# Kernel tuning notes

Measured on AMD Instinct MI355X. Metric: run time of the kernel, lower is better.

The kernel has to match this reference:

```python
import jax, jax.numpy as jnp
import numpy as np

NUM_EMBED = 8192
EMBED_DIM = 256


def setup_inputs() -> dict:
    key = jax.random.key(0)
    k1, k2 = jax.random.split(key)
    input_data = jax.random.normal(k1, (32, EMBED_DIM, 32, 32), dtype=jnp.float32)
    codebook = jax.random.normal(k2, (NUM_EMBED, EMBED_DIM), dtype=jnp.float32)
    return {"input_data": input_data, "codebook": codebook}


def reference(input_data, codebook):
    N, C, H, W = input_data.shape
    # NCHW -> NHWC -> [N*H*W, C]
    data = jnp.transpose(input_data, (0, 2, 3, 1)).reshape(-1, C)
    dist = (
        jnp.sum(data * data, axis=1, keepdims=True)          # [T, 1]
        - 2.0 * jnp.einsum("tc,kc->tk", data, codebook)      # [T, K]
        + jnp.sum(codebook * codebook, axis=1)[None, :]       # [1, K]
    )
    embed_ind = jnp.argmin(dist, axis=1)                      # [T]
    quantize = codebook[embed_ind]                            # [T, C] gather
    quantize_detach = data + jax.lax.stop_gradient(quantize - data)
    return quantize, quantize_detach, data
```

## Files before the change

kernel.cpp:

```cpp
#include <hip/hip_runtime.h>
#include <stdint.h>


#define T_TOT 32768
#define K_TOT 8192
#define CD    256
#define SPLITS 4
#define NSPLIT 2048
#define MT    64
#define NTI   32

typedef _Float16 h8 __attribute__((ext_vector_type(8)));
typedef _Float16 h4 __attribute__((ext_vector_type(4)));
typedef _Float16 h2 __attribute__((ext_vector_type(2)));
typedef float f4 __attribute__((ext_vector_type(4)));
typedef unsigned long long u64;
typedef unsigned int u32;

#define WS_AP    0u
#define WS_BP    16777216u
#define WS_E2    20971520u
#define WS_E2B   21004288u
#define WS_CAND  21037056u
#define WS_NEED  23265280u

__device__ __forceinline__ u64 shfl_xor_u64(u64 v, int off, int w) {
  unsigned lo = (unsigned)v, hi = (unsigned)(v >> 32);
  lo = __shfl_xor(lo, off, w);
  hi = __shfl_xor(hi, off, w);
  return ((u64)hi << 32) | lo;
}
__device__ __forceinline__ u64 umin64(u64 a, u64 b) { return a < b ? a : b; }
__device__ __forceinline__ u64 umax64(u64 a, u64 b) { return a < b ? b : a; }
__device__ __forceinline__ u32 umin32(u32 a, u32 b) { return a < b ? a : b; }
__device__ __forceinline__ u32 umax32(u32 a, u32 b) { return a < b ? b : a; }



__global__ __launch_bounds__(256) void cvt_data_kernel(
    const float* __restrict__ in, _Float16* __restrict__ Ap) {
  __shared__ float Ds[32][257];
  const int tid = threadIdx.x;
  const int t0 = blockIdx.x * 32;
  const int nbase = (t0 >> 10) << 18;
  const int tin = t0 & 1023;
  #pragma unroll 8
  for (int p = 0; p < 32; ++p) {
    const int lin = p * 256 + tid;
    const int cc = lin >> 5, tt = lin & 31;
    Ds[tt][cc] = in[nbase + cc * 1024 + tin + tt];
  }
  __syncthreads();
  const u64 g0 = (u64)(t0 >> 4);
  #pragma unroll
  for (int p = 0; p < 4; ++p) {
    const int id = p * 256 + tid;
    const int gl = id >> 9, kk = (id >> 6) & 7, l = id & 63;
    const int row = gl * 16 + (l & 15);
    const int c0 = kk * 32 + (l >> 4) * 8;
    h8 hv;
    #pragma unroll
    for (int j = 0; j < 8; ++j) hv[j] = (_Float16)(-Ds[row][c0 + j]);
    *(h8*)(Ap + ((g0 + (u64)gl) * 8 + kk) * 512 + (u64)l * 8) = hv;
  }
}

__global__ __launch_bounds__(256) void cvt_cb_kernel(
    const float* __restrict__ cb, _Float16* __restrict__ Bp,
    float* __restrict__ e2, float* __restrict__ e2b) {
  __shared__ float Cs[16][260];
  const int tid = threadIdx.x;
  const int g = blockIdx.x;
  #pragma unroll
  for (int r = 0; r < 16; ++r)
    Cs[r][tid] = cb[((u64)g * 16 + r) * 256 + tid];
  __syncthreads();
  const int w = tid >> 6, lane = tid & 63;
  #pragma unroll
  for (int rr = 0; rr < 4; ++rr) {
    const int row = w * 4 + rr;
    const float4 v = *(const float4*)&Cs[row][lane * 4];
    float s = v.x * v.x + v.y * v.y + v.z * v.z + v.w * v.w;
    #pragma unroll
    for (int off = 32; off >= 1; off >>= 1) s += __shfl_xor(s, off, 64);
    if (lane == 0) {
      e2[g * 16 + row] = s;
      e2b[g * 16 + row] = 0.5f * s + 256.0f;
    }
  }
  #pragma unroll
  for (int p = 0; p < 2; ++p) {
    const int id = p * 256 + tid;
    const int kk = id >> 6, l = id & 63;
    const int row = l & 15, c0 = kk * 32 + (l >> 4) * 8;
    h8 hv;
    #pragma unroll
    for (int j = 0; j < 8; ++j) hv[j] = (_Float16)Cs[row][c0 + j];
    *(h8*)(Bp + ((u64)g * 8 + kk) * 512 + (u64)l * 8) = hv;
  }
}

__global__ __launch_bounds__(256, 2) void screen_kernel(
    const _Float16* __restrict__ Ap, const _Float16* __restrict__ Bp,
    const float* __restrict__ e2b, u64* __restrict__ cand) {
  __shared__ u64 mbuf[4][64][2];

  const int tid = threadIdx.x;
  const int lane = tid & 63;
  const int w = tid >> 6;
  const int q = lane >> 4;
  const int c15 = lane & 15;

  const int bm = blockIdx.x & 511;
  const int split = blockIdx.x >> 9;
  const int t0 = bm * MT;
  const int n0s = split * NSPLIT;

  const h8* ap = (const h8*)Ap + (u64)(t0 >> 4) * 512 + lane;
  h8 af[4][8];
  #pragma unroll
  for (int mi = 0; mi < 4; ++mi)
    #pragma unroll
    for (int kk = 0; kk < 8; ++kk)
      af[mi][kk] = ap[(mi * 8 + kk) * 64];

  const h8* bp = (const h8*)Bp + ((u64)(n0s >> 4) + (u64)w) * 512 + lane;
  h8 bf[8];
  #pragma unroll
  for (int kk = 0; kk < 8; ++kk) bf[kk] = bp[kk * 64];

  const float* e2p = e2b + n0s + w * 16 + c15;
  float ev = e2p[0];

  u32 m1[16], m2[16];
  #pragma unroll
  for (int r = 0; r < 16; ++r) { m1[r] = 0xffffffffu; m2[r] = 0xffffffffu; }

  #pragma unroll 1
  for (int nt = 0; nt < NTI; ++nt) {
    const int ntn = (nt < NTI - 1) ? nt + 1 : nt;
    const float evn = e2p[ntn * 64];
    const h8* bn = bp + (u64)ntn * 2048;
    f4 acc[4];
    #pragma unroll
    for (int mi = 0; mi < 4; ++mi) acc[mi] = (f4){ev, ev, ev, ev};
    #pragma unroll
    for (int kk = 0; kk < 8; ++kk) {
      const h8 b = bf[kk];
      acc[0] = __builtin_amdgcn_mfma_f32_16x16x32_f16(af[0][kk], b, acc[0], 0, 0, 0);
      acc[1] = __builtin_amdgcn_mfma_f32_16x16x32_f16(af[1][kk], b, acc[1], 0, 0, 0);
      acc[2] = __builtin_amdgcn_mfma_f32_16x16x32_f16(af[2][kk], b, acc[2], 0, 0, 0);
      acc[3] = __builtin_amdgcn_mfma_f32_16x16x32_f16(af[3][kk], b, acc[3], 0, 0, 0);
      bf[kk] = bn[kk * 64];
    }
    #pragma unroll
    for (int mi = 0; mi < 4; ++mi)
      #pragma unroll
      for (int reg = 0; reg < 4; ++reg) {
        const int r = mi * 4 + reg;
        const u32 k = (__float_as_uint(acc[mi][reg]) & ~63u) | (u32)nt;
        const u32 t = umax32(m1[r], k);
        m1[r] = umin32(m1[r], k);
        m2[r] = umin32(m2[r], t);
      }
    ev = evn;
  }

  u64 P1[16], P2[16];
  #pragma unroll
  for (int r = 0; r < 16; ++r) {
    const u32 l1 = m1[r] & 63u, l2 = m2[r] & 63u;
    const u32 col1 = (u32)(n0s + (int)l1 * 64 + w * 16 + c15);
    const u32 col2 = (u32)(n0s + (int)l2 * 64 + w * 16 + c15);
    P1[r] = ((u64)m1[r] << 32) | col1;
    P2[r] = ((u64)m2[r] << 32) | col2;
  }
  #pragma unroll
  for (int st = 1; st < 16; st <<= 1) {
    #pragma unroll
    for (int r = 0; r < 16; ++r) {
      const u64 o1 = shfl_xor_u64(P1[r], st, 16);
      const u64 o2 = shfl_xor_u64(P2[r], st, 16);
      const u64 n1 = umin64(P1[r], o1);
      const u64 hi = umax64(P1[r], o1);
      P2[r] = umin64(hi, umin64(P2[r], o2));
      P1[r] = n1;
    }
  }
  if (c15 == 0) {
    #pragma unroll
    for (int r = 0; r < 16; ++r) {
      const int mi = r >> 2, reg = r & 3;
      const int row = mi * 16 + q * 4 + reg;
      mbuf[w][row][0] = P1[r];
      mbuf[w][row][1] = P2[r];
    }
  }
  __syncthreads();
  if (tid < 64) {
    const u64 a1 = mbuf[0][tid][0], a2 = mbuf[0][tid][1];
    const u64 b1 = mbuf[1][tid][0], b2 = mbuf[1][tid][1];
    const u64 c1 = mbuf[2][tid][0], c2 = mbuf[2][tid][1];
    const u64 d1 = mbuf[3][tid][0], d2 = mbuf[3][tid][1];
    const u64 x1 = umin64(a1, b1);
    const u64 x2 = umin64(umax64(a1, b1), umin64(a2, b2));
    const u64 y1 = umin64(c1, d1);
    const u64 y2 = umin64(umax64(c1, d1), umin64(c2, d2));
    const u64 n1 = umin64(x1, y1);
    const u64 n2 = umin64(umax64(x1, y1), umin64(x2, y2));
    cand[(u64)(t0 + tid) * 8 + split * 2 + 0] = n1;
    cand[(u64)(t0 + tid) * 8 + split * 2 + 1] = n2;
  }
}

__global__ __launch_bounds__(256) void rescore_output_kernel(
    const float* __restrict__ in, const float* __restrict__ cb,
    const float* __restrict__ e2, const u64* __restrict__ cand,
    float* __restrict__ out) {
  __shared__ __align__(16) float Ds[32][260];
  __shared__ int idxs[32];
  const int tid = threadIdx.x;
  const int t0 = blockIdx.x * 32;
  const int nbase = (t0 >> 10) << 18;
  const int tin = t0 & 1023;
  #pragma unroll 8
  for (int p = 0; p < 32; ++p) {
    const int lin = p * 256 + tid;
    const int cc = lin >> 5, tt = lin & 31;
    Ds[tt][cc] = in[nbase + cc * 1024 + tin + tt];
  }
  __syncthreads();
  const int w = tid >> 6, lane = tid & 63;
  for (int s = 0; s < 8; ++s) {
    const int tt = w * 8 + s;
    const int t = t0 + tt;
    int colv = 0;
    if (lane < 8) colv = (int)(u32)cand[(u64)t * 8 + lane];
    const float4 x = *(const float4*)&Ds[tt][lane * 4];
    float bestd = 1e30f; int bestc = 0x7fffffff;
    #pragma unroll
    for (int j = 0; j < 8; ++j) {
      const int col = __shfl(colv, j, 64);
      const float4 e = *(const float4*)(cb + (u64)col * CD + lane * 4);
      float p4 = x.x * e.x + x.y * e.y + x.z * e.z + x.w * e.w;
      #pragma unroll
      for (int off = 32; off >= 1; off >>= 1) p4 += __shfl_xor(p4, off, 64);
      const float d = e2[col] - 2.0f * p4;
      if (d < bestd || (d == bestd && col < bestc)) { bestd = d; bestc = col; }
    }
    if (lane == 0) idxs[tt] = bestc;
  }
  __syncthreads();
  float* out1 = out;
  float* out2 = out + 8388608;
  float* out3 = out + 16777216;
  for (int tt = 0; tt < 32; ++tt) {
    const float d = Ds[tt][tid];
    const int k = idxs[tt];
    const float qv = cb[k * CD + tid];
    const float qd = d + (qv - d);
    const int o = (t0 + tt) * CD + tid;
    out1[o] = qv;
    out2[o] = qd;
    out3[o] = d;
  }
}


__global__ __launch_bounds__(256) void norms_kernel(const float* __restrict__ in,
                                                    const float* __restrict__ cb,
                                                    float* __restrict__ e2,
                                                    float* __restrict__ x2) {
  const int b = blockIdx.x;
  const int tid = threadIdx.x;
  if (b < 2048) {
    const int wave = tid >> 6, lane = tid & 63;
    const int row = b * 4 + wave;
    const float4 v = *(const float4*)(cb + row * CD + lane * 4);
    float s = v.x * v.x + v.y * v.y + v.z * v.z + v.w * v.w;
    #pragma unroll
    for (int off = 32; off >= 1; off >>= 1) s += __shfl_down(s, off, 64);
    if (lane == 0) e2[row] = s;
  } else {
    const int t = (b - 2048) * 256 + tid;
    const float* p = in + ((t >> 10) << 18) + (t & 1023);
    float s = 0.f;
    #pragma unroll 8
    for (int c = 0; c < CD; ++c) { const float v = p[c << 10]; s += v * v; }
    x2[t] = s;
  }
}

__global__ __launch_bounds__(256) void dist_argmin_kernel(
    const float* __restrict__ in, const float* __restrict__ cb,
    const float* __restrict__ e2, const float* __restrict__ x2,
    u64* __restrict__ packed) {
  __shared__ __align__(16) float As_[32][128];
  __shared__ __align__(16) float Bs_[32][128];
  const int tid = threadIdx.x;
  const int tx = tid & 15, ty = tid >> 4;
  const int tb = blockIdx.x & 255;
  const int ks = blockIdx.x >> 8;
  const int t0 = tb * 128;
  const int nbase = (t0 >> 10) << 18;
  const int tin = t0 & 1023;
  float xi[8];
  #pragma unroll
  for (int i = 0; i < 8; ++i)
    xi[i] = x2[t0 + ty * 4 + (i & 3) + ((i >> 2) << 6)];
  u64 best[8];
  #pragma unroll
  for (int i = 0; i < 8; ++i) best[i] = ~0ull;
  for (int kt = 0; kt < 32; ++kt) {
    const int k0 = ks * 4096 + kt * 128;
    float acc[8][8];
    #pragma unroll
    for (int i = 0; i < 8; ++i)
      #pragma unroll
      for (int j = 0; j < 8; ++j) acc[i][j] = 0.f;
    float ej[8];
    #pragma unroll
    for (int j = 0; j < 8; ++j)
      ej[j] = e2[k0 + tx * 4 + (j & 3) + ((j >> 2) << 6)];
    for (int ch = 0; ch < 8; ++ch) {
      const int c0 = ch * 32;
      #pragma unroll
      for (int p = 0; p < 4; ++p) {
        const int l = p * 1024 + tid * 4;
        const int cc = l >> 7, tt = l & 127;
        *(float4*)&As_[cc][tt] =
            *(const float4*)(in + nbase + (c0 + cc) * 1024 + tin + tt);
      }
      #pragma unroll
      for (int p = 0; p < 4; ++p) {
        const int ix = p * 256 + tid;
        const int kk = ix >> 3, cs = (ix & 7) * 4;
        const float4 v = *(const float4*)(cb + (k0 + kk) * CD + c0 + cs);
        Bs_[cs + 0][kk] = v.x; Bs_[cs + 1][kk] = v.y;
        Bs_[cs + 2][kk] = v.z; Bs_[cs + 3][kk] = v.w;
      }
      __syncthreads();
      #pragma unroll
      for (int cc = 0; cc < 32; ++cc) {
        const float4 a0 = *(const float4*)&As_[cc][ty * 4];
        const float4 a1 = *(const float4*)&As_[cc][64 + ty * 4];
        const float4 b0 = *(const float4*)&Bs_[cc][tx * 4];
        const float4 b1 = *(const float4*)&Bs_[cc][64 + tx * 4];
        const float a[8]  = {a0.x, a0.y, a0.z, a0.w, a1.x, a1.y, a1.z, a1.w};
        const float bb[8] = {b0.x, b0.y, b0.z, b0.w, b1.x, b1.y, b1.z, b1.w};
        #pragma unroll
        for (int i = 0; i < 8; ++i)
          #pragma unroll
          for (int j = 0; j < 8; ++j)
            acc[i][j] += a[i] * bb[j];
      }
      __syncthreads();
    }
    #pragma unroll
    for (int i = 0; i < 8; ++i) {
      u64 m = best[i];
      #pragma unroll
      for (int j = 0; j < 8; ++j) {
        const float dist = (xi[i] - 2.0f * acc[i][j]) + ej[j];
        const int kidx = k0 + tx * 4 + (j & 3) + ((j >> 2) << 6);
        const u64 pk = ((u64)__float_as_uint(dist) << 32) | (unsigned)kidx;
        m = pk < m ? pk : m;
      }
      best[i] = m;
    }
  }
  #pragma unroll
  for (int i = 0; i < 8; ++i) {
    u64 m = best[i];
    #pragma unroll
    for (int off = 8; off >= 1; off >>= 1) {
      const u64 o = shfl_xor_u64(m, off, 16);
      m = o < m ? o : m;
    }
    if (tx == 0)
      atomicMin(&packed[t0 + ty * 4 + (i & 3) + ((i >> 2) << 6)], m);
  }
}

__global__ __launch_bounds__(256) void output_kernel(
    const float* __restrict__ in, const float* __restrict__ cb,
    const u64* __restrict__ packed, float* __restrict__ out) {
  __shared__ float Ds[32][257];
  __shared__ int idxs[32];
  const int tid = threadIdx.x;
  const int t0 = blockIdx.x * 32;
  const int nbase = (t0 >> 10) << 18;
  const int tin = t0 & 1023;
  if (tid < 32) idxs[tid] = (int)(packed[t0 + tid] & 0xffffffffull);
  #pragma unroll 8
  for (int p = 0; p < 32; ++p) {
    const int lin = p * 256 + tid;
    const int cc = lin >> 5, tt = lin & 31;
    Ds[tt][cc] = in[nbase + cc * 1024 + tin + tt];
  }
  __syncthreads();
  float* out1 = out;
  float* out2 = out + 8388608;
  float* out3 = out + 16777216;
  for (int tt = 0; tt < 32; ++tt) {
    const float d = Ds[tt][tid];
    const int k = idxs[tt];
    const float q = cb[k * CD + tid];
    const float qd = d + (q - d);
    const int o = (t0 + tt) * CD + tid;
    out1[o] = q;
    out2[o] = qd;
    out3[o] = d;
  }
}

extern "C" void kernel_launch(void* const* d_in, const int* in_sizes, int n_in,
                              void* d_out, int out_size, void* d_ws, size_t ws_size,
                              hipStream_t stream) {
  const float* in = (const float*)d_in[0];
  const float* cb = (const float*)d_in[1];
  float* out = (float*)d_out;

  if (ws_size >= WS_NEED) {
    _Float16* Ap = (_Float16*)((char*)d_ws + WS_AP);
    _Float16* Bp = (_Float16*)((char*)d_ws + WS_BP);
    float* e2  = (float*)((char*)d_ws + WS_E2);
    float* e2b = (float*)((char*)d_ws + WS_E2B);
    u64* cand  = (u64*)((char*)d_ws + WS_CAND);

    cvt_data_kernel<<<T_TOT / 32, 256, 0, stream>>>(in, Ap);
    cvt_cb_kernel<<<K_TOT / 16, 256, 0, stream>>>(cb, Bp, e2, e2b);
    screen_kernel<<<(T_TOT / MT) * SPLITS, 256, 0, stream>>>(Ap, Bp, e2b, cand);
    rescore_output_kernel<<<T_TOT / 32, 256, 0, stream>>>(in, cb, e2, cand, out);
  } else {
    u64* packed = (u64*)d_ws;
    float* e2 = (float*)((char*)d_ws + 262144);
    float* x2 = (float*)((char*)d_ws + 294912);
    hipMemsetAsync(packed, 0xFF, T_TOT * sizeof(u64), stream);
    norms_kernel<<<2176, 256, 0, stream>>>(in, cb, e2, x2);
    dist_argmin_kernel<<<512, 256, 0, stream>>>(in, cb, e2, x2, packed);
    output_kernel<<<T_TOT / 32, 256, 0, stream>>>(in, cb, packed, out);
  }
}
```

Measured before the change: 404.4 us.

## Stage codebook tiles via async global_load_lds double buffering in screen kernel

The screen kernel now loads codebook B fragments and the e2 bias into LDS with global_load_lds. Each wave double-buffers its 16-column tile and prefetches two iterations ahead, replacing the direct register prefetch from global memory. Block indices are also remapped so the four splits of neighbouring row tiles run adjacently, which should improve L2 reuse of A and B. The change adds LDS traffic and hand-placed waitcnt and sched_barrier instructions, and it reuses the B buffer for the final reduction. Correctness depends on the manual vmcnt accounting being right.

```diff
diff --git a/kernel.cpp b/kernel.cpp
--- a/kernel.cpp
+++ b/kernel.cpp
@@ -34,6 +34,19 @@
 __device__ __forceinline__ u64 umax64(u64 a, u64 b) { return a < b ? b : a; }
 __device__ __forceinline__ u32 umin32(u32 a, u32 b) { return a < b ? a : b; }
 __device__ __forceinline__ u32 umax32(u32 a, u32 b) { return a < b ? b : a; }
+
+__device__ __forceinline__ void gll16(const void* g, void* l) {
+  __builtin_amdgcn_global_load_lds(
+      (const __attribute__((address_space(1))) void*)g,
+      (__attribute__((address_space(3))) void*)l, 16, 0, 0);
+}
+
+__device__ __forceinline__ void stage_b(const _Float16* __restrict__ gsrc,
+                                        _Float16* ldst, int lane) {
+  #pragma unroll
+  for (int kk = 0; kk < 8; ++kk)
+    gll16(gsrc + kk * 512 + lane * 8, ldst + kk * 512);
+}
 
 
 
@@ -103,7 +116,8 @@
 __global__ __launch_bounds__(256, 2) void screen_kernel(
     const _Float16* __restrict__ Ap, const _Float16* __restrict__ Bp,
     const float* __restrict__ e2b, u64* __restrict__ cand) {
-  __shared__ u64 mbuf[4][64][2];
+  __shared__ __align__(16) _Float16 bsm[4][2][4096];
+  __shared__ __align__(16) float e2s[2048];
 
   const int tid = threadIdx.x;
   const int lane = tid & 63;
@@ -111,8 +125,10 @@
   const int q = lane >> 4;
   const int c15 = lane & 15;
 
-  const int bm = blockIdx.x & 511;
-  const int split = blockIdx.x >> 9;
+  const int x = blockIdx.x & 7;
+  const int m = blockIdx.x >> 3;
+  const int split = x >> 1;
+  const int bm = m * 2 + (x & 1);
   const int t0 = bm * MT;
   const int n0s = split * NSPLIT;
 
@@ -124,35 +140,44 @@
     for (int kk = 0; kk < 8; ++kk)
       af[mi][kk] = ap[(mi * 8 + kk) * 64];
 
-  const h8* bp = (const h8*)Bp + ((u64)(n0s >> 4) + (u64)w) * 512 + lane;
-  h8 bf[8];
-  #pragma unroll
-  for (int kk = 0; kk < 8; ++kk) bf[kk] = bp[kk * 64];
-
-  const float* e2p = e2b + n0s + w * 16 + c15;
-  float ev = e2p[0];
+  const _Float16* bg = Bp + ((u64)(n0s >> 4) + (u64)w) * 4096;
+  stage_b(bg, &bsm[w][0][0], lane);
+  stage_b(bg + 16384, &bsm[w][1][0], lane);
+  gll16(e2b + n0s + w * 512 + lane * 4, e2s + w * 512);
+  gll16(e2b + n0s + w * 512 + 256 + lane * 4, e2s + w * 512 + 256);
 
   u32 m1[16], m2[16];
   #pragma unroll
   for (int r = 0; r < 16; ++r) { m1[r] = 0xffffffffu; m2[r] = 0xffffffffu; }
 
-  #pragma unroll 1
+  __syncthreads();
+
+  #pragma unroll 2
   for (int nt = 0; nt < NTI; ++nt) {
-    const int ntn = (nt < NTI - 1) ? nt + 1 : nt;
-    const float evn = e2p[ntn * 64];
-    const h8* bn = bp + (u64)ntn * 2048;
+    asm volatile("s_waitcnt vmcnt(8)" ::: "memory");
+    _Float16* slot = &bsm[w][nt & 1][0];
+    const float ev = e2s[nt * 64 + w * 16 + c15];
+    h8 bf[8];
+    #pragma unroll
+    for (int kk = 0; kk < 8; ++kk)
+      bf[kk] = *(const h8*)(slot + kk * 512 + lane * 8);
+
     f4 acc[4];
     #pragma unroll
     for (int mi = 0; mi < 4; ++mi) acc[mi] = (f4){ev, ev, ev, ev};
     #pragma unroll
     for (int kk = 0; kk < 8; ++kk) {
-      const h8 b = bf[kk];
-      acc[0] = __builtin_amdgcn_mfma_f32_16x16x32_f16(af[0][kk], b, acc[0], 0, 0, 0);
-      acc[1] = __builtin_amdgcn_mfma_f32_16x16x32_f16(af[1][kk], b, acc[1], 0, 0, 0);
-      acc[2] = __builtin_amdgcn_mfma_f32_16x16x32_f16(af[2][kk], b, acc[2], 0, 0, 0);
-      acc[3] = __builtin_amdgcn_mfma_f32_16x16x32_f16(af[3][kk], b, acc[3], 0, 0, 0);
-      bf[kk] = bn[kk * 64];
-    }
+      acc[0] = __builtin_amdgcn_mfma_f32_16x16x32_f16(af[0][kk], bf[kk], acc[0], 0, 0, 0);
+      acc[1] = __builtin_amdgcn_mfma_f32_16x16x32_f16(af[1][kk], bf[kk], acc[1], 0, 0, 0);
+      acc[2] = __builtin_amdgcn_mfma_f32_16x16x32_f16(af[2][kk], bf[kk], acc[2], 0, 0, 0);
+      acc[3] = __builtin_amdgcn_mfma_f32_16x16x32_f16(af[3][kk], bf[kk], acc[3], 0, 0, 0);
+    }
+
+    asm volatile("s_waitcnt lgkmcnt(0)" ::: "memory");
+    __builtin_amdgcn_sched_barrier(0);
+    const int g2 = (nt + 2 < NTI) ? nt + 2 : NTI - 1;
+    stage_b(bg + (u64)g2 * 16384, slot, lane);
+
     #pragma unroll
     for (int mi = 0; mi < 4; ++mi)
       #pragma unroll
@@ -163,7 +188,6 @@
         m1[r] = umin32(m1[r], k);
         m2[r] = umin32(m2[r], t);
       }
-    ev = evn;
   }
 
   u64 P1[16], P2[16];
@@ -187,21 +211,23 @@
       P1[r] = n1;
     }
   }
+  __syncthreads();
+  u64* mb = (u64*)&bsm[0][0][0];
   if (c15 == 0) {
     #pragma unroll
     for (int r = 0; r < 16; ++r) {
       const int mi = r >> 2, reg = r & 3;
       const int row = mi * 16 + q * 4 + reg;
-      mbuf[w][row][0] = P1[r];
-      mbuf[w][row][1] = P2[r];
+      mb[(w * 64 + row) * 2 + 0] = P1[r];
+      mb[(w * 64 + row) * 2 + 1] = P2[r];
     }
   }
   __syncthreads();
   if (tid < 64) {
-    const u64 a1 = mbuf[0][tid][0], a2 = mbuf[0][tid][1];
-    const u64 b1 = mbuf[1][tid][0], b2 = mbuf[1][tid][1];
-    const u64 c1 = mbuf[2][tid][0], c2 = mbuf[2][tid][1];
-    const u64 d1 = mbuf[3][tid][0], d2 = mbuf[3][tid][1];
+    const u64 a1 = mb[(0 * 64 + tid) * 2], a2 = mb[(0 * 64 + tid) * 2 + 1];
+    const u64 b1 = mb[(1 * 64 + tid) * 2], b2 = mb[(1 * 64 + tid) * 2 + 1];
+    const u64 c1 = mb[(2 * 64 + tid) * 2], c2 = mb[(2 * 64 + tid) * 2 + 1];
+    const u64 d1 = mb[(3 * 64 + tid) * 2], d2 = mb[(3 * 64 + tid) * 2 + 1];
     const u64 x1 = umin64(a1, b1);
     const u64 x2 = umin64(umax64(a1, b1), umin64(a2, b2));
     const u64 y1 = umin64(c1, d1);
```

After: 331.3 us. 1.22x faster.
